# Kernel optimization log

Hardware: AMD Instinct MI355X
Metric: run time of the kernel (lower is better)

The kernel has to match this reference:

```python
import jax, jax.numpy as jnp
import numpy as np

B, S, H = 2, 2048, 1024
NUM_HEADS = 16


def setup_inputs() -> dict:
    key = jax.random.key(0)
    ks = jax.random.split(key, 5)
    scale = 1.0 / np.sqrt(H)
    x = jax.random.normal(ks[0], (B, S, H), dtype=jnp.float32)
    W_qkv = jax.random.normal(ks[1], (3 * H, H), dtype=jnp.float32) * scale
    b_qkv = jax.random.normal(ks[2], (3 * H,), dtype=jnp.float32) * 0.02
    W_o = jax.random.normal(ks[3], (H, H), dtype=jnp.float32) * scale
    b_o = jax.random.normal(ks[4], (H,), dtype=jnp.float32) * 0.02
    return {"x": x, "W_qkv": W_qkv, "b_qkv": b_qkv, "W_o": W_o, "b_o": b_o}


def reference(x, W_qkv, b_qkv, W_o, b_o):
    b, s, h = x.shape
    n = NUM_HEADS
    d_head = h // n
    # QKV projection (torch Linear: x @ W.T + b), then chunk into Q, K, V
    qkv = x @ W_qkv.T + b_qkv                      # [b, s, 3h]
    Q, K, V = jnp.split(qkv, 3, axis=-1)           # each [b, s, h]
    # split heads: b s (n d) -> b n s d
    Q = Q.reshape(b, s, n, d_head).transpose(0, 2, 1, 3)
    K = K.reshape(b, s, n, d_head).transpose(0, 2, 1, 3)
    V = V.reshape(b, s, n, d_head).transpose(0, 2, 1, 3)
    # scores, causal mask, scale (mask before/after scale is equivalent: -inf stays -inf)
    scores = jnp.einsum('bnqd,bnkd->bnqk', Q, K) / jnp.sqrt(jnp.float32(d_head))
    causal = jnp.tril(jnp.ones((s, s), dtype=bool))  # True = keep
    scores = jnp.where(causal, scores, -jnp.inf)
    A = jax.nn.softmax(scores, axis=-1)
    AV = jnp.einsum('bnqk,bnkd->bnqd', A, V)
    out = AV.transpose(0, 2, 1, 3).reshape(b, s, h)  # merge heads
    return out @ W_o.T + b_o
```

## Files before the change

### kernel.cpp

```cpp
#include <hip/hip_runtime.h>
#include <cstdint>
#include <cstddef>

#define BATCH 2
#define SEQ   2048
#define HID   1024
#define NHEAD 16
#define DHEAD 64
#define QKV_N 3072
#define NTOK  4096

typedef __attribute__((ext_vector_type(4))) float f32x4;
typedef __attribute__((ext_vector_type(8))) short bf16x8;

#define QSCL 0.18033688011112042f

__device__ inline unsigned short f2bf(float f) {
    union { float f; unsigned int u; } v; v.f = f;
    unsigned int u = v.u;
    unsigned int r = (u + 0x7fffu + ((u >> 16) & 1u)) >> 16;
    return (unsigned short)r;
}

__device__ __forceinline__ void gload_lds16(const void* g, void* l) {
    __builtin_amdgcn_global_load_lds(
        (const __attribute__((address_space(1))) void*)g,
        (__attribute__((address_space(3))) void*)l, 16, 0, 0);
}

__global__ void cast_f32_bf16(const float* __restrict__ in, unsigned short* __restrict__ out, int n4) {
    int i = blockIdx.x * blockDim.x + threadIdx.x;
    if (i >= n4) return;
    float4 v = reinterpret_cast<const float4*>(in)[i];
    ushort4 o;
    o.x = f2bf(v.x); o.y = f2bf(v.y); o.z = f2bf(v.z); o.w = f2bf(v.w);
    reinterpret_cast<ushort4*>(out)[i] = o;
}

template<int BN, int OUT_MODE>
__global__ __launch_bounds__(256) void gemm_bt(const short* __restrict__ A,
                                               const short* __restrict__ B,
                                               const float* __restrict__ bias,
                                               void* __restrict__ Cout,
                                               int M, int N, int K) {
    constexpr int WTN = BN / 2;
    constexpr int NJ  = WTN / 16;
    constexpr int NBC = BN / 64;

    __shared__ short sA[2][128 * 32];
    __shared__ short sB[2][BN * 32];

    const int tid  = threadIdx.x;
    const int lane = tid & 63;
    const int wave = tid >> 6;
    const int wm = wave >> 1, wn = wave & 1;

    const int nwg = gridDim.x;
    const int swz = (blockIdx.x & 7) * (nwg >> 3) + (blockIdx.x >> 3);
    const int tiles_n = N / BN;
    const int m0 = (swz / tiles_n) * 128;
    const int n0 = (swz % tiles_n) * BN;

    f32x4 acc[4][NJ];
    #pragma unroll
    for (int i = 0; i < 4; ++i)
        #pragma unroll
        for (int j = 0; j < NJ; ++j) acc[i][j] = (f32x4){0.f, 0.f, 0.f, 0.f};

    const int r = lane & 15;
    const int G = lane >> 4;

    #define GSTAGE(kt_, buf_)                                                          \
        {                                                                              \
            _Pragma("unroll")                                                          \
            for (int i = 0; i < 2; ++i) {                                              \
                int ga = (i * 4 + wave) * 64 + lane;                                   \
                int row = ga >> 2, gcol = (ga & 3) ^ (row & 3);                        \
                gload_lds16(A + (size_t)(m0 + row) * K + (kt_) + gcol * 8,             \
                            &sA[buf_][(i * 4 + wave) * 512]);                          \
            }                                                                          \
            _Pragma("unroll")                                                          \
            for (int i = 0; i < NBC; ++i) {                                            \
                int gb = (i * 4 + wave) * 64 + lane;                                   \
                int row = gb >> 2, gcol = (gb & 3) ^ (row & 3);                        \
                gload_lds16(B + (size_t)(n0 + row) * K + (kt_) + gcol * 8,             \
                            &sB[buf_][(i * 4 + wave) * 512]);                          \
            }                                                                          \
        }

    GSTAGE(0, 0);
    __syncthreads();
    int cur = 0;

    const int nsteps = K >> 5;
    for (int ks = 0; ks < nsteps; ++ks) {
        if (ks + 1 < nsteps) GSTAGE((ks + 1) * 32, cur ^ 1);

        const int sg = G ^ (r & 3);
        bf16x8 af[4], bfr[NJ];
        #pragma unroll
        for (int i = 0; i < 4; ++i) {
            int row = wm * 64 + i * 16 + r;
            af[i] = *reinterpret_cast<const bf16x8*>(&sA[cur][row * 32 + sg * 8]);
        }
        #pragma unroll
        for (int j = 0; j < NJ; ++j) {
            int row = wn * WTN + j * 16 + r;
            bfr[j] = *reinterpret_cast<const bf16x8*>(&sB[cur][row * 32 + sg * 8]);
        }
        #pragma unroll
        for (int i = 0; i < 4; ++i)
            #pragma unroll
            for (int j = 0; j < NJ; ++j)
                acc[i][j] = __builtin_amdgcn_mfma_f32_16x16x32_bf16(af[i], bfr[j], acc[i][j], 0, 0, 0);

        __syncthreads();
        cur ^= 1;
    }
    #undef GSTAGE

    const int col_l = lane & 15;
    const int row_g = (lane >> 4) * 4;
    #pragma unroll
    for (int i = 0; i < 4; ++i) {
        #pragma unroll
        for (int j = 0; j < NJ; ++j) {
            int nn = n0 + wn * WTN + j * 16 + col_l;
            float bv = bias[nn];
            float scl = (OUT_MODE == 2 && nn < HID) ? QSCL : 1.0f;
            #pragma unroll
            for (int reg = 0; reg < 4; ++reg) {
                int mm = m0 + wm * 64 + i * 16 + row_g + reg;
                float v = (acc[i][j][reg] + bv) * scl;
                if (OUT_MODE == 0) {
                    reinterpret_cast<float*>(Cout)[(size_t)mm * N + nn] = v;
                } else {
                    reinterpret_cast<unsigned short*>(Cout)[(size_t)mm * N + nn] = f2bf(v);
                }
            }
        }
    }
}

#define TLDP 72
__global__ __launch_bounds__(256) void transpose_v(const short* __restrict__ qkv,
                                                   short* __restrict__ vT) {
    const int st = blockIdx.x;
    const int bh = blockIdx.y;
    const int b  = bh >> 4, h = bh & 15;
    __shared__ short ld[64 * TLDP];
    const int tid = threadIdx.x;

    #pragma unroll
    for (int i = 0; i < 2; ++i) {
        int idx = i * 256 + tid;
        int row = idx >> 3, c = idx & 7;
        int4 v = *reinterpret_cast<const int4*>(
            qkv + ((size_t)(b * SEQ + st * 64 + row)) * QKV_N + 2 * HID + h * DHEAD + c * 8);
        *reinterpret_cast<int4*>(&ld[row * TLDP + c * 8]) = v;
    }
    __syncthreads();
    #pragma unroll
    for (int i = 0; i < 4; ++i) {
        int idx = i * 256 + tid;
        int d = idx >> 4, sc = idx & 15;
        ushort4 o;
        o.x = (unsigned short)ld[(sc * 4 + 0) * TLDP + d];
        o.y = (unsigned short)ld[(sc * 4 + 1) * TLDP + d];
        o.z = (unsigned short)ld[(sc * 4 + 2) * TLDP + d];
        o.w = (unsigned short)ld[(sc * 4 + 3) * TLDP + d];
        *reinterpret_cast<ushort4*>(&vT[((size_t)(bh * DHEAD + d)) * SEQ + st * 64 + sc * 4]) = o;
    }
}

__global__ __launch_bounds__(64, 2) void attn_fwd(const short* __restrict__ qkv,
                                                  const short* __restrict__ vT,
                                                  short* __restrict__ av) {
    const int bid = blockIdx.x;
    const int qb  = 63 - (bid >> 5);
    const int bh  = bid & 31;
    const int b   = bh >> 4;
    const int h   = bh & 15;

    __shared__ short sK [2][32 * 64];
    __shared__ short sVT[2][64 * 32];

    const int lane = threadIdx.x;
    const int r    = lane & 15;
    const int G    = lane >> 4;
    const int row_g = G * 4;

    const int qbw = qb * 32;

    bf16x8 qf[2][2];
    #pragma unroll
    for (int mi = 0; mi < 2; ++mi) {
        const short* Qg = qkv + ((size_t)(b * SEQ + qbw + mi * 16 + r)) * QKV_N + h * DHEAD;
        qf[mi][0] = *reinterpret_cast<const bf16x8*>(Qg + G * 8);
        qf[mi][1] = *reinterpret_cast<const bf16x8*>(Qg + 32 + G * 8);
    }

    f32x4 oacc[2][4];
    f32x4 oL[2];
    #pragma unroll
    for (int mi = 0; mi < 2; ++mi) {
        oL[mi] = (f32x4){0.f, 0.f, 0.f, 0.f};
        #pragma unroll
        for (int dg = 0; dg < 4; ++dg) oacc[mi][dg] = (f32x4){0.f, 0.f, 0.f, 0.f};
    }

    bf16x8 ones;
    #pragma unroll
    for (int e = 0; e < 8; ++e) ones[e] = (short)0x3f80;

    const int krow_ = lane >> 3, kgr_ = lane & 7;
    const int vrow_ = lane >> 2, vgr_ = lane & 3;

    #define STAGE(kv0_, buf_)                                                              \
        {                                                                                  \
            _Pragma("unroll")                                                              \
            for (int i = 0; i < 4; ++i) {                                                  \
                int row  = i * 8 + krow_;                                                  \
                int srcg = kgr_ ^ (row & 7);                                               \
                gload_lds16(qkv + (size_t)(b * SEQ + (kv0_) + row) * QKV_N                 \
                                + HID + h * DHEAD + srcg * 8,                              \
                            &sK[buf_][i * 512]);                                           \
            }                                                                              \
            _Pragma("unroll")                                                              \
            for (int i = 0; i < 4; ++i) {                                                  \
                int row  = i * 16 + vrow_;                                                 \
                int srcg = vgr_ ^ (row & 3);                                               \
                gload_lds16(vT + (size_t)(bh * DHEAD + row) * SEQ + (kv0_) + srcg * 8,     \
                            &sVT[buf_][i * 512]);                                          \
            }                                                                              \
        }

    STAGE(0, 0);
    int cur = 0;

    for (int t = 0; t <= qb; ++t) {
        if (t < qb) {
            STAGE((t + 1) * 32, cur ^ 1);
            asm volatile("s_waitcnt vmcnt(8)" ::: "memory");
        } else {
            asm volatile("s_waitcnt vmcnt(0)" ::: "memory");
        }
        __builtin_amdgcn_sched_barrier(0);

        bf16x8 kb[2][2];
        #pragma unroll
        for (int g = 0; g < 2; ++g) {
            int row = g * 16 + r;
            kb[g][0] = *reinterpret_cast<const bf16x8*>(&sK[cur][row * 64 + ((0 + G) ^ (row & 7)) * 8]);
            kb[g][1] = *reinterpret_cast<const bf16x8*>(&sK[cur][row * 64 + ((4 + G) ^ (row & 7)) * 8]);
        }
        bf16x8 vb[4];
        #pragma unroll
        for (int dg = 0; dg < 4; ++dg) {
            int row_d = dg * 16 + r;
            int rm = row_d & 3;
            int eo = (G & 1) * 4;
            int glo = (G >> 1) ^ rm;
            int ghi = (2 + (G >> 1)) ^ rm;
            uint2 lo = *reinterpret_cast<const uint2*>(&sVT[cur][row_d * 32 + glo * 8 + eo]);
            uint2 hi = *reinterpret_cast<const uint2*>(&sVT[cur][row_d * 32 + ghi * 8 + eo]);
            int4 f; f.x = lo.x; f.y = lo.y; f.z = hi.x; f.w = hi.y;
            __builtin_memcpy(&vb[dg], &f, 16);
        }

        const bool diag = (t == qb);

        #pragma unroll
        for (int mi = 0; mi < 2; ++mi) {
            f32x4 s[2];
            #pragma unroll
            for (int g = 0; g < 2; ++g) {
                f32x4 z = (f32x4){0.f, 0.f, 0.f, 0.f};
                z = __builtin_amdgcn_mfma_f32_16x16x32_bf16(kb[g][0], qf[mi][0], z, 0, 0, 0);
                z = __builtin_amdgcn_mfma_f32_16x16x32_bf16(kb[g][1], qf[mi][1], z, 0, 0, 0);
                s[g] = z;
            }
            if (diag) {
                int ql = mi * 16 + r;
                #pragma unroll
                for (int g = 0; g < 2; ++g) {
                    #pragma unroll
                    for (int reg = 0; reg < 4; ++reg) {
                        int kvl = g * 16 + row_g + reg;
                        if (kvl > ql) s[g][reg] = -30000.f;
                    }
                }
            }
            unsigned int w0, w1, w2, w3;
            {
                float p0 = __builtin_amdgcn_exp2f(s[0][0]);
                float p1 = __builtin_amdgcn_exp2f(s[0][1]);
                float p2 = __builtin_amdgcn_exp2f(s[0][2]);
                float p3 = __builtin_amdgcn_exp2f(s[0][3]);
                float p4 = __builtin_amdgcn_exp2f(s[1][0]);
                float p5 = __builtin_amdgcn_exp2f(s[1][1]);
                float p6 = __builtin_amdgcn_exp2f(s[1][2]);
                float p7 = __builtin_amdgcn_exp2f(s[1][3]);
                w0 = (unsigned int)f2bf(p0) | ((unsigned int)f2bf(p1) << 16);
                w1 = (unsigned int)f2bf(p2) | ((unsigned int)f2bf(p3) << 16);
                w2 = (unsigned int)f2bf(p4) | ((unsigned int)f2bf(p5) << 16);
                w3 = (unsigned int)f2bf(p6) | ((unsigned int)f2bf(p7) << 16);
            }
            bf16x8 pb;
            { int4 f; f.x = (int)w0; f.y = (int)w1; f.z = (int)w2; f.w = (int)w3;
              __builtin_memcpy(&pb, &f, 16); }

            #pragma unroll
            for (int dg = 0; dg < 4; ++dg)
                oacc[mi][dg] = __builtin_amdgcn_mfma_f32_16x16x32_bf16(vb[dg], pb, oacc[mi][dg], 0, 0, 0);
            oL[mi] = __builtin_amdgcn_mfma_f32_16x16x32_bf16(ones, pb, oL[mi], 0, 0, 0);
        }

        cur ^= 1;
    }

    #pragma unroll
    for (int mi = 0; mi < 2; ++mi) {
        float il = 1.0f / oL[mi][0];
        size_t tok = (size_t)(b * SEQ + qbw + mi * 16 + r);
        #pragma unroll
        for (int dg = 0; dg < 4; ++dg) {
            ushort4 o;
            o.x = f2bf(oacc[mi][dg][0] * il);
            o.y = f2bf(oacc[mi][dg][1] * il);
            o.z = f2bf(oacc[mi][dg][2] * il);
            o.w = f2bf(oacc[mi][dg][3] * il);
            *reinterpret_cast<ushort4*>(&av[tok * HID + h * DHEAD + dg * 16 + row_g]) = o;
        }
    }
}

extern "C" void kernel_launch(void* const* d_in, const int* in_sizes, int n_in,
                              void* d_out, int out_size, void* d_ws, size_t ws_size,
                              hipStream_t stream) {
    const float* x     = (const float*)d_in[0];
    const float* W_qkv = (const float*)d_in[1];
    const float* b_qkv = (const float*)d_in[2];
    const float* W_o   = (const float*)d_in[3];
    const float* b_o   = (const float*)d_in[4];
    float* out = (float*)d_out;

    const int n_x    = NTOK * HID;
    const int n_wqkv = QKV_N * HID;
    const int n_wo   = HID * HID;
    const int n_qkv  = NTOK * QKV_N;
    const int n_av   = NTOK * HID;

    short* xb    = (short*)d_ws;
    short* wqkvb = xb + n_x;
    short* wob   = wqkvb + n_wqkv;
    short* qkv   = wob + n_wo;
    short* av    = qkv + n_qkv;
    short* vT    = av + n_av;

    cast_f32_bf16<<<n_x / 1024,    256, 0, stream>>>(x,     (unsigned short*)xb,    n_x / 4);
    cast_f32_bf16<<<n_wqkv / 1024, 256, 0, stream>>>(W_qkv, (unsigned short*)wqkvb, n_wqkv / 4);
    cast_f32_bf16<<<n_wo / 1024,   256, 0, stream>>>(W_o,   (unsigned short*)wob,   n_wo / 4);

    gemm_bt<128, 2><<<(NTOK / 128) * (QKV_N / 128), 256, 0, stream>>>(
        xb, wqkvb, b_qkv, (void*)qkv, NTOK, QKV_N, HID);

    transpose_v<<<dim3(SEQ / 64, BATCH * NHEAD), 256, 0, stream>>>(qkv, vT);

    attn_fwd<<<2048, 64, 0, stream>>>(qkv, vT, av);

    gemm_bt<64, 0><<<(NTOK / 128) * (HID / 64), 256, 0, stream>>>(
        av, wob, b_o, (void*)out, NTOK, HID, HID);
}
```

Before: 129.4 us.

## Split attention KV loop across four waves per block with LDS reduction

The attention kernel now runs four waves per block. Each wave handles every fourth KV tile for the same 32-query block, using its own double-buffered LDS tiles. Partial outputs and row sums are then combined serially through a shared-memory buffer before normalisation and store. This is meant to shorten the serial KV loop for long causal rows and raise parallelism, at the cost of more LDS per block, a serialized four-step reduction with barriers, and idle waves on short rows.

```diff
diff --git a/kernel.cpp b/kernel.cpp
--- a/kernel.cpp
+++ b/kernel.cpp
@@ -173,19 +173,22 @@
     }
 }
 
-__global__ __launch_bounds__(64, 2) void attn_fwd(const short* __restrict__ qkv,
-                                                  const short* __restrict__ vT,
-                                                  short* __restrict__ av) {
+__global__ __launch_bounds__(256, 2) void attn_fwd(const short* __restrict__ qkv,
+                                                   const short* __restrict__ vT,
+                                                   short* __restrict__ av) {
     const int bid = blockIdx.x;
     const int qb  = 63 - (bid >> 5);
     const int bh  = bid & 31;
     const int b   = bh >> 4;
     const int h   = bh & 15;
 
-    __shared__ short sK [2][32 * 64];
-    __shared__ short sVT[2][64 * 32];
-
-    const int lane = threadIdx.x;
+    __shared__ short sK [4][2][32 * 64];
+    __shared__ short sVT[4][2][64 * 32];
+    __shared__ float comb[32][68];
+
+    const int tid  = threadIdx.x;
+    const int lane = tid & 63;
+    const int wave = tid >> 6;
     const int r    = lane & 15;
     const int G    = lane >> 4;
     const int row_g = G * 4;
@@ -224,113 +227,154 @@
                 int srcg = kgr_ ^ (row & 7);                                               \
                 gload_lds16(qkv + (size_t)(b * SEQ + (kv0_) + row) * QKV_N                 \
                                 + HID + h * DHEAD + srcg * 8,                              \
-                            &sK[buf_][i * 512]);                                           \
+                            &sK[wave][buf_][i * 512]);                                     \
             }                                                                              \
             _Pragma("unroll")                                                              \
             for (int i = 0; i < 4; ++i) {                                                  \
                 int row  = i * 16 + vrow_;                                                 \
                 int srcg = vgr_ ^ (row & 3);                                               \
                 gload_lds16(vT + (size_t)(bh * DHEAD + row) * SEQ + (kv0_) + srcg * 8,     \
-                            &sVT[buf_][i * 512]);                                          \
+                            &sVT[wave][buf_][i * 512]);                                    \
             }                                                                              \
         }
 
-    STAGE(0, 0);
-    int cur = 0;
-
-    for (int t = 0; t <= qb; ++t) {
-        if (t < qb) {
-            STAGE((t + 1) * 32, cur ^ 1);
-            asm volatile("s_waitcnt vmcnt(8)" ::: "memory");
-        } else {
-            asm volatile("s_waitcnt vmcnt(0)" ::: "memory");
-        }
-        __builtin_amdgcn_sched_barrier(0);
-
-        bf16x8 kb[2][2];
-        #pragma unroll
-        for (int g = 0; g < 2; ++g) {
-            int row = g * 16 + r;
-            kb[g][0] = *reinterpret_cast<const bf16x8*>(&sK[cur][row * 64 + ((0 + G) ^ (row & 7)) * 8]);
-            kb[g][1] = *reinterpret_cast<const bf16x8*>(&sK[cur][row * 64 + ((4 + G) ^ (row & 7)) * 8]);
-        }
-        bf16x8 vb[4];
-        #pragma unroll
-        for (int dg = 0; dg < 4; ++dg) {
-            int row_d = dg * 16 + r;
-            int rm = row_d & 3;
-            int eo = (G & 1) * 4;
-            int glo = (G >> 1) ^ rm;
-            int ghi = (2 + (G >> 1)) ^ rm;
-            uint2 lo = *reinterpret_cast<const uint2*>(&sVT[cur][row_d * 32 + glo * 8 + eo]);
-            uint2 hi = *reinterpret_cast<const uint2*>(&sVT[cur][row_d * 32 + ghi * 8 + eo]);
-            int4 f; f.x = lo.x; f.y = lo.y; f.z = hi.x; f.w = hi.y;
-            __builtin_memcpy(&vb[dg], &f, 16);
-        }
-
-        const bool diag = (t == qb);
-
-        #pragma unroll
-        for (int mi = 0; mi < 2; ++mi) {
-            f32x4 s[2];
+    if (wave <= qb) {
+        STAGE(wave * 32, 0);
+        int cur = 0;
+        for (int t = wave; t <= qb; t += 4) {
+            if (t + 4 <= qb) {
+                STAGE((t + 4) * 32, cur ^ 1);
+                asm volatile("s_waitcnt vmcnt(8)" ::: "memory");
+            } else {
+                asm volatile("s_waitcnt vmcnt(0)" ::: "memory");
+            }
+            __builtin_amdgcn_sched_barrier(0);
+
+            bf16x8 kb[2][2];
             #pragma unroll
             for (int g = 0; g < 2; ++g) {
-                f32x4 z = (f32x4){0.f, 0.f, 0.f, 0.f};
-                z = __builtin_amdgcn_mfma_f32_16x16x32_bf16(kb[g][0], qf[mi][0], z, 0, 0, 0);
-                z = __builtin_amdgcn_mfma_f32_16x16x32_bf16(kb[g][1], qf[mi][1], z, 0, 0, 0);
-                s[g] = z;
-            }
-            if (diag) {
-                int ql = mi * 16 + r;
+                int row = g * 16 + r;
+                kb[g][0] = *reinterpret_cast<const bf16x8*>(&sK[wave][cur][row * 64 + ((0 + G) ^ (row & 7)) * 8]);
+                kb[g][1] = *reinterpret_cast<const bf16x8*>(&sK[wave][cur][row * 64 + ((4 + G) ^ (row & 7)) * 8]);
+            }
+            bf16x8 vb[4];
+            #pragma unroll
+            for (int dg = 0; dg < 4; ++dg) {
+                int row_d = dg * 16 + r;
+                int rm = row_d & 3;
+                int eo = (G & 1) * 4;
+                int glo = (G >> 1) ^ rm;
+                int ghi = (2 + (G >> 1)) ^ rm;
+                uint2 lo = *reinterpret_cast<const uint2*>(&sVT[wave][cur][row_d * 32 + glo * 8 + eo]);
+                uint2 hi = *reinterpret_cast<const uint2*>(&sVT[wave][cur][row_d * 32 + ghi * 8 + eo]);
+                int4 f; f.x = lo.x; f.y = lo.y; f.z = hi.x; f.w = hi.y;
+                __builtin_memcpy(&vb[dg], &f, 16);
+            }
+
+            const bool diag = (t == qb);
+
+            #pragma unroll
+            for (int mi = 0; mi < 2; ++mi) {
+                f32x4 s[2];
                 #pragma unroll
                 for (int g = 0; g < 2; ++g) {
+                    f32x4 z = (f32x4){0.f, 0.f, 0.f, 0.f};
+                    z = __builtin_amdgcn_mfma_f32_16x16x32_bf16(kb[g][0], qf[mi][0], z, 0, 0, 0);
+                    z = __builtin_amdgcn_mfma_f32_16x16x32_bf16(kb[g][1], qf[mi][1], z, 0, 0, 0);
+                    s[g] = z;
+                }
+                if (diag) {
+                    int ql = mi * 16 + r;
                     #pragma unroll
-                    for (int reg = 0; reg < 4; ++reg) {
-                        int kvl = g * 16 + row_g + reg;
-                        if (kvl > ql) s[g][reg] = -30000.f;
+                    for (int g = 0; g < 2; ++g) {
+                        #pragma unroll
+                        for (int reg = 0; reg < 4; ++reg) {
+                            int kvl = g * 16 + row_g + reg;
+                            if (kvl > ql) s[g][reg] = -30000.f;
+                        }
                     }
                 }
-            }
-            unsigned int w0, w1, w2, w3;
-            {
-                float p0 = __builtin_amdgcn_exp2f(s[0][0]);
-                float p1 = __builtin_amdgcn_exp2f(s[0][1]);
-                float p2 = __builtin_amdgcn_exp2f(s[0][2]);
-                float p3 = __builtin_amdgcn_exp2f(s[0][3]);
-                float p4 = __builtin_amdgcn_exp2f(s[1][0]);
-                float p5 = __builtin_amdgcn_exp2f(s[1][1]);
-                float p6 = __builtin_amdgcn_exp2f(s[1][2]);
-                float p7 = __builtin_amdgcn_exp2f(s[1][3]);
-                w0 = (unsigned int)f2bf(p0) | ((unsigned int)f2bf(p1) << 16);
-                w1 = (unsigned int)f2bf(p2) | ((unsigned int)f2bf(p3) << 16);
-                w2 = (unsigned int)f2bf(p4) | ((unsigned int)f2bf(p5) << 16);
-                w3 = (unsigned int)f2bf(p6) | ((unsigned int)f2bf(p7) << 16);
-            }
-            bf16x8 pb;
-            { int4 f; f.x = (int)w0; f.y = (int)w1; f.z = (int)w2; f.w = (int)w3;
-              __builtin_memcpy(&pb, &f, 16); }
-
+                unsigned int w0, w1, w2, w3;
+                {
+                    float p0 = __builtin_amdgcn_exp2f(s[0][0]);
+                    float p1 = __builtin_amdgcn_exp2f(s[0][1]);
+                    float p2 = __builtin_amdgcn_exp2f(s[0][2]);
+                    float p3 = __builtin_amdgcn_exp2f(s[0][3]);
+                    float p4 = __builtin_amdgcn_exp2f(s[1][0]);
+                    float p5 = __builtin_amdgcn_exp2f(s[1][1]);
+                    float p6 = __builtin_amdgcn_exp2f(s[1][2]);
+                    float p7 = __builtin_amdgcn_exp2f(s[1][3]);
+                    w0 = (unsigned int)f2bf(p0) | ((unsigned int)f2bf(p1) << 16);
+                    w1 = (unsigned int)f2bf(p2) | ((unsigned int)f2bf(p3) << 16);
+                    w2 = (unsigned int)f2bf(p4) | ((unsigned int)f2bf(p5) << 16);
+                    w3 = (unsigned int)f2bf(p6) | ((unsigned int)f2bf(p7) << 16);
+                }
+                bf16x8 pb;
+                { int4 f; f.x = (int)w0; f.y = (int)w1; f.z = (int)w2; f.w = (int)w3;
+                  __builtin_memcpy(&pb, &f, 16); }
+
+                #pragma unroll
+                for (int dg = 0; dg < 4; ++dg)
+                    oacc[mi][dg] = __builtin_amdgcn_mfma_f32_16x16x32_bf16(vb[dg], pb, oacc[mi][dg], 0, 0, 0);
+                oL[mi] = __builtin_amdgcn_mfma_f32_16x16x32_bf16(ones, pb, oL[mi], 0, 0, 0);
+            }
+
+            cur ^= 1;
+        }
+    }
+
+    __syncthreads();
+    if (wave == 0) {
+        #pragma unroll
+        for (int mi = 0; mi < 2; ++mi) {
             #pragma unroll
             for (int dg = 0; dg < 4; ++dg)
-                oacc[mi][dg] = __builtin_amdgcn_mfma_f32_16x16x32_bf16(vb[dg], pb, oacc[mi][dg], 0, 0, 0);
-            oL[mi] = __builtin_amdgcn_mfma_f32_16x16x32_bf16(ones, pb, oL[mi], 0, 0, 0);
-        }
-
-        cur ^= 1;
-    }
-
-    #pragma unroll
-    for (int mi = 0; mi < 2; ++mi) {
-        float il = 1.0f / oL[mi][0];
-        size_t tok = (size_t)(b * SEQ + qbw + mi * 16 + r);
-        #pragma unroll
-        for (int dg = 0; dg < 4; ++dg) {
-            ushort4 o;
-            o.x = f2bf(oacc[mi][dg][0] * il);
-            o.y = f2bf(oacc[mi][dg][1] * il);
-            o.z = f2bf(oacc[mi][dg][2] * il);
-            o.w = f2bf(oacc[mi][dg][3] * il);
-            *reinterpret_cast<ushort4*>(&av[tok * HID + h * DHEAD + dg * 16 + row_g]) = o;
+                *reinterpret_cast<f32x4*>(&comb[mi * 16 + r][dg * 16 + row_g]) = oacc[mi][dg];
+            if (G == 0) comb[mi * 16 + r][64] = oL[mi][0];
+        }
+    }
+    __syncthreads();
+    if (wave == 1) {
+        #pragma unroll
+        for (int mi = 0; mi < 2; ++mi) {
+            #pragma unroll
+            for (int dg = 0; dg < 4; ++dg) {
+                f32x4 c = *reinterpret_cast<f32x4*>(&comb[mi * 16 + r][dg * 16 + row_g]);
+                *reinterpret_cast<f32x4*>(&comb[mi * 16 + r][dg * 16 + row_g]) = c + oacc[mi][dg];
+            }
+            if (G == 0) comb[mi * 16 + r][64] += oL[mi][0];
+        }
+    }
+    __syncthreads();
+    if (wave == 2) {
+        #pragma unroll
+        for (int mi = 0; mi < 2; ++mi) {
+            #pragma unroll
+            for (int dg = 0; dg < 4; ++dg) {
+                f32x4 c = *reinterpret_cast<f32x4*>(&comb[mi * 16 + r][dg * 16 + row_g]);
+                *reinterpret_cast<f32x4*>(&comb[mi * 16 + r][dg * 16 + row_g]) = c + oacc[mi][dg];
+            }
+            if (G == 0) comb[mi * 16 + r][64] += oL[mi][0];
+        }
+    }
+    __syncthreads();
+    if (wave == 3) {
+        #pragma unroll
+        for (int mi = 0; mi < 2; ++mi) {
+            float l = comb[mi * 16 + r][64] + oL[mi][0];
+            float il = 1.0f / l;
+            size_t tok = (size_t)(b * SEQ + qbw + mi * 16 + r);
+            #pragma unroll
+            for (int dg = 0; dg < 4; ++dg) {
+                f32x4 tot = *reinterpret_cast<f32x4*>(&comb[mi * 16 + r][dg * 16 + row_g]);
+                tot = tot + oacc[mi][dg];
+                ushort4 o;
+                o.x = f2bf(tot[0] * il);
+                o.y = f2bf(tot[1] * il);
+                o.z = f2bf(tot[2] * il);
+                o.w = f2bf(tot[3] * il);
+                *reinterpret_cast<ushort4*>(&av[tok * HID + h * DHEAD + dg * 16 + row_g]) = o;
+            }
         }
     }
 }
@@ -367,7 +411,7 @@
 
     transpose_v<<<dim3(SEQ / 64, BATCH * NHEAD), 256, 0, stream>>>(qkv, vT);
 
-    attn_fwd<<<2048, 64, 0, stream>>>(qkv, vT, av);
+    attn_fwd<<<2048, 256, 0, stream>>>(qkv, vT, av);
 
     gemm_bt<64, 0><<<(NTOK / 128) * (HID / 64), 256, 0, stream>>>(
         av, wob, b_o, (void*)out, NTOK, HID, HID);
```

Measured after the change: 121.8 us. -5.8%, faster.

## Split attention KV loop across two waves, pre-pack V in MFMA fragment layout

Applied to the files above, without the earlier changes.

The attention kernel now launches two waves per block. Each wave handles alternating 32-key tiles, and their partial output and row-sum accumulators are combined through shared memory at the end. K and V fragments are loaded straight from global memory into registers, with no LDS staging and no double buffering. The V transpose kernel writes a new packed layout so that each lane's MFMA operand is one contiguous 16-byte load. The aim is more parallelism per block and less LDS traffic, at the cost of losing the explicit prefetch pipelining and adding a cross-wave reduction.

```diff
diff --git a/kernel.cpp b/kernel.cpp
--- a/kernel.cpp
+++ b/kernel.cpp
@@ -144,7 +144,7 @@
 
 #define TLDP 72
 __global__ __launch_bounds__(256) void transpose_v(const short* __restrict__ qkv,
-                                                   short* __restrict__ vT) {
+                                                   short* __restrict__ vP) {
     const int st = blockIdx.x;
     const int bh = blockIdx.y;
     const int b  = bh >> 4, h = bh & 15;
@@ -161,31 +161,42 @@
     }
     __syncthreads();
     #pragma unroll
-    for (int i = 0; i < 4; ++i) {
-        int idx = i * 256 + tid;
-        int d = idx >> 4, sc = idx & 15;
-        ushort4 o;
-        o.x = (unsigned short)ld[(sc * 4 + 0) * TLDP + d];
-        o.y = (unsigned short)ld[(sc * 4 + 1) * TLDP + d];
-        o.z = (unsigned short)ld[(sc * 4 + 2) * TLDP + d];
-        o.w = (unsigned short)ld[(sc * 4 + 3) * TLDP + d];
-        *reinterpret_cast<ushort4*>(&vT[((size_t)(bh * DHEAD + d)) * SEQ + st * 64 + sc * 4]) = o;
-    }
-}
-
-__global__ __launch_bounds__(64, 2) void attn_fwd(const short* __restrict__ qkv,
-                                                  const short* __restrict__ vT,
-                                                  short* __restrict__ av) {
+    for (int i = 0; i < 2; ++i) {
+        int u  = i * 256 + tid;
+        int Tp = u >> 8;
+        int d  = (u >> 2) & 63;
+        int p  = u & 3;
+        int b0 = Tp * 32 + 4 * p;
+        int b1 = b0 + 16;
+        ushort4 o0, o1;
+        o0.x = (unsigned short)ld[(b0 + 0) * TLDP + d];
+        o0.y = (unsigned short)ld[(b0 + 1) * TLDP + d];
+        o0.z = (unsigned short)ld[(b0 + 2) * TLDP + d];
+        o0.w = (unsigned short)ld[(b0 + 3) * TLDP + d];
+        o1.x = (unsigned short)ld[(b1 + 0) * TLDP + d];
+        o1.y = (unsigned short)ld[(b1 + 1) * TLDP + d];
+        o1.z = (unsigned short)ld[(b1 + 2) * TLDP + d];
+        o1.w = (unsigned short)ld[(b1 + 3) * TLDP + d];
+        size_t out = ((size_t)((bh * 64 + st * 2 + Tp) * 64 + d)) * 32 + p * 8;
+        *reinterpret_cast<ushort4*>(&vP[out])     = o0;
+        *reinterpret_cast<ushort4*>(&vP[out + 4]) = o1;
+    }
+}
+
+__global__ __launch_bounds__(128) void attn_fwd(const short* __restrict__ qkv,
+                                                const short* __restrict__ vP,
+                                                short* __restrict__ av) {
     const int bid = blockIdx.x;
     const int qb  = 63 - (bid >> 5);
     const int bh  = bid & 31;
     const int b   = bh >> 4;
     const int h   = bh & 15;
 
-    __shared__ short sK [2][32 * 64];
-    __shared__ short sVT[2][64 * 32];
-
-    const int lane = threadIdx.x;
+    __shared__ float comb[32][68];
+
+    const int tid  = threadIdx.x;
+    const int lane = tid & 63;
+    const int wave = tid >> 6;
     const int r    = lane & 15;
     const int G    = lane >> 4;
     const int row_g = G * 4;
@@ -213,60 +224,34 @@
     #pragma unroll
     for (int e = 0; e < 8; ++e) ones[e] = (short)0x3f80;
 
-    const int krow_ = lane >> 3, kgr_ = lane & 7;
-    const int vrow_ = lane >> 2, vgr_ = lane & 3;
-
-    #define STAGE(kv0_, buf_)                                                              \
-        {                                                                                  \
-            _Pragma("unroll")                                                              \
-            for (int i = 0; i < 4; ++i) {                                                  \
-                int row  = i * 8 + krow_;                                                  \
-                int srcg = kgr_ ^ (row & 7);                                               \
-                gload_lds16(qkv + (size_t)(b * SEQ + (kv0_) + row) * QKV_N                 \
-                                + HID + h * DHEAD + srcg * 8,                              \
-                            &sK[buf_][i * 512]);                                           \
-            }                                                                              \
-            _Pragma("unroll")                                                              \
-            for (int i = 0; i < 4; ++i) {                                                  \
-                int row  = i * 16 + vrow_;                                                 \
-                int srcg = vgr_ ^ (row & 3);                                               \
-                gload_lds16(vT + (size_t)(bh * DHEAD + row) * SEQ + (kv0_) + srcg * 8,     \
-                            &sVT[buf_][i * 512]);                                          \
-            }                                                                              \
-        }
-
-    STAGE(0, 0);
-    int cur = 0;
-
-    for (int t = 0; t <= qb; ++t) {
-        if (t < qb) {
-            STAGE((t + 1) * 32, cur ^ 1);
-            asm volatile("s_waitcnt vmcnt(8)" ::: "memory");
-        } else {
-            asm volatile("s_waitcnt vmcnt(0)" ::: "memory");
-        }
-        __builtin_amdgcn_sched_barrier(0);
-
-        bf16x8 kb[2][2];
-        #pragma unroll
-        for (int g = 0; g < 2; ++g) {
-            int row = g * 16 + r;
-            kb[g][0] = *reinterpret_cast<const bf16x8*>(&sK[cur][row * 64 + ((0 + G) ^ (row & 7)) * 8]);
-            kb[g][1] = *reinterpret_cast<const bf16x8*>(&sK[cur][row * 64 + ((4 + G) ^ (row & 7)) * 8]);
-        }
-        bf16x8 vb[4];
-        #pragma unroll
-        for (int dg = 0; dg < 4; ++dg) {
-            int row_d = dg * 16 + r;
-            int rm = row_d & 3;
-            int eo = (G & 1) * 4;
-            int glo = (G >> 1) ^ rm;
-            int ghi = (2 + (G >> 1)) ^ rm;
-            uint2 lo = *reinterpret_cast<const uint2*>(&sVT[cur][row_d * 32 + glo * 8 + eo]);
-            uint2 hi = *reinterpret_cast<const uint2*>(&sVT[cur][row_d * 32 + ghi * 8 + eo]);
-            int4 f; f.x = lo.x; f.y = lo.y; f.z = hi.x; f.w = hi.y;
-            __builtin_memcpy(&vb[dg], &f, 16);
-        }
+    const short* kp0 = qkv + (size_t)(b * SEQ) * QKV_N + HID + h * DHEAD;
+    const short* vp0 = vP + (size_t)(bh * 64) * 2048;
+    const int koff0 = r * QKV_N + G * 8;
+    const int koff1 = (16 + r) * QKV_N + G * 8;
+    const int voffb = r * 32 + G * 8;
+
+    for (int t = wave; t <= qb; t += 2) {
+        const short* kpt = kp0 + (size_t)t * 32 * QKV_N;
+        const short* vpt = vp0 + (size_t)t * 2048;
+
+        int4 k00 = *reinterpret_cast<const int4*>(kpt + koff0);
+        int4 k01 = *reinterpret_cast<const int4*>(kpt + koff0 + 32);
+        int4 k10 = *reinterpret_cast<const int4*>(kpt + koff1);
+        int4 k11 = *reinterpret_cast<const int4*>(kpt + koff1 + 32);
+        int4 v0 = *reinterpret_cast<const int4*>(vpt + voffb);
+        int4 v1 = *reinterpret_cast<const int4*>(vpt + voffb + 16 * 32);
+        int4 v2 = *reinterpret_cast<const int4*>(vpt + voffb + 32 * 32);
+        int4 v3 = *reinterpret_cast<const int4*>(vpt + voffb + 48 * 32);
+
+        bf16x8 kb[2][2], vb[4];
+        __builtin_memcpy(&kb[0][0], &k00, 16);
+        __builtin_memcpy(&kb[0][1], &k01, 16);
+        __builtin_memcpy(&kb[1][0], &k10, 16);
+        __builtin_memcpy(&kb[1][1], &k11, 16);
+        __builtin_memcpy(&vb[0], &v0, 16);
+        __builtin_memcpy(&vb[1], &v1, 16);
+        __builtin_memcpy(&vb[2], &v2, 16);
+        __builtin_memcpy(&vb[3], &v3, 16);
 
         const bool diag = (t == qb);
 
@@ -315,22 +300,35 @@
                 oacc[mi][dg] = __builtin_amdgcn_mfma_f32_16x16x32_bf16(vb[dg], pb, oacc[mi][dg], 0, 0, 0);
             oL[mi] = __builtin_amdgcn_mfma_f32_16x16x32_bf16(ones, pb, oL[mi], 0, 0, 0);
         }
-
-        cur ^= 1;
-    }
-
-    #pragma unroll
-    for (int mi = 0; mi < 2; ++mi) {
-        float il = 1.0f / oL[mi][0];
-        size_t tok = (size_t)(b * SEQ + qbw + mi * 16 + r);
-        #pragma unroll
-        for (int dg = 0; dg < 4; ++dg) {
-            ushort4 o;
-            o.x = f2bf(oacc[mi][dg][0] * il);
-            o.y = f2bf(oacc[mi][dg][1] * il);
-            o.z = f2bf(oacc[mi][dg][2] * il);
-            o.w = f2bf(oacc[mi][dg][3] * il);
-            *reinterpret_cast<ushort4*>(&av[tok * HID + h * DHEAD + dg * 16 + row_g]) = o;
+    }
+
+    if (wave == 0) {
+        #pragma unroll
+        for (int mi = 0; mi < 2; ++mi) {
+            #pragma unroll
+            for (int dg = 0; dg < 4; ++dg)
+                *reinterpret_cast<f32x4*>(&comb[mi * 16 + r][dg * 16 + row_g]) = oacc[mi][dg];
+            if (G == 0) comb[mi * 16 + r][64] = oL[mi][0];
+        }
+    }
+    __syncthreads();
+    if (wave == 1) {
+        #pragma unroll
+        for (int mi = 0; mi < 2; ++mi) {
+            float l = comb[mi * 16 + r][64] + oL[mi][0];
+            float il = 1.0f / l;
+            size_t tok = (size_t)(b * SEQ + qbw + mi * 16 + r);
+            #pragma unroll
+            for (int dg = 0; dg < 4; ++dg) {
+                f32x4 tot = *reinterpret_cast<f32x4*>(&comb[mi * 16 + r][dg * 16 + row_g]);
+                tot = tot + oacc[mi][dg];
+                ushort4 o;
+                o.x = f2bf(tot[0] * il);
+                o.y = f2bf(tot[1] * il);
+                o.z = f2bf(tot[2] * il);
+                o.w = f2bf(tot[3] * il);
+                *reinterpret_cast<ushort4*>(&av[tok * HID + h * DHEAD + dg * 16 + row_g]) = o;
+            }
         }
     }
 }
@@ -356,7 +354,7 @@
     short* wob   = wqkvb + n_wqkv;
     short* qkv   = wob + n_wo;
     short* av    = qkv + n_qkv;
-    short* vT    = av + n_av;
+    short* vP    = av + n_av;
 
     cast_f32_bf16<<<n_x / 1024,    256, 0, stream>>>(x,     (unsigned short*)xb,    n_x / 4);
     cast_f32_bf16<<<n_wqkv / 1024, 256, 0, stream>>>(W_qkv, (unsigned short*)wqkvb, n_wqkv / 4);
@@ -365,9 +363,9 @@
     gemm_bt<128, 2><<<(NTOK / 128) * (QKV_N / 128), 256, 0, stream>>>(
         xb, wqkvb, b_qkv, (void*)qkv, NTOK, QKV_N, HID);
 
-    transpose_v<<<dim3(SEQ / 64, BATCH * NHEAD), 256, 0, stream>>>(qkv, vT);
-
-    attn_fwd<<<2048, 64, 0, stream>>>(qkv, vT, av);
+    transpose_v<<<dim3(SEQ / 64, BATCH * NHEAD), 256, 0, stream>>>(qkv, vP);
+
+    attn_fwd<<<2048, 128, 0, stream>>>(qkv, vP, av);
 
     gemm_bt<64, 0><<<(NTOK / 128) * (HID / 64), 256, 0, stream>>>(
         av, wob, b_o, (void*)out, NTOK, HID, HID);
```

Result: no change. 128.5 us (-0.7%).
